# Kernel optimization log

Measured on AMD Instinct MI355X. Metric: run time of the kernel, lower is better.

Reference implementation:

```python
import jax, jax.numpy as jnp
from jax import lax
import numpy as np

B, L, D_MODEL = 4, 2048, 1024
D_STATE, D_CONV, EXPAND = 16, 4, 2
D_INNER = EXPAND * D_MODEL          # 2048
DT_RANK = D_MODEL // 16             # 64
LN_EPS = 1e-5


def setup_inputs() -> dict:
    key = jax.random.key(0)
    ks = jax.random.split(key, 8)
    s = 0.02
    # S4D-real init for A_log, as in Mamba
    A_init = jnp.tile(jnp.arange(1, D_STATE + 1, dtype=jnp.float32), (D_INNER, 1))
    return {
        "x": jax.random.normal(ks[0], (B, L, D_MODEL), jnp.float32),
        "ln_g": jnp.ones((D_MODEL,), jnp.float32),
        "ln_b": jnp.zeros((D_MODEL,), jnp.float32),
        "W_in": jax.random.normal(ks[1], (D_MODEL, 2 * D_INNER), jnp.float32) * s,
        "conv_w": jax.random.normal(ks[2], (D_INNER, D_CONV), jnp.float32) * s,
        "conv_b": jnp.zeros((D_INNER,), jnp.float32),
        "W_x": jax.random.normal(ks[3], (D_INNER, DT_RANK + 2 * D_STATE), jnp.float32) * s,
        "W_dt": jax.random.normal(ks[4], (DT_RANK, D_INNER), jnp.float32) * s,
        "b_dt": jnp.full((D_INNER,), -4.6, jnp.float32),  # softplus(b_dt) ~ 0.01
        "A_log": jnp.log(A_init),
        "Dskip": jnp.ones((D_INNER,), jnp.float32),
        "W_out": jax.random.normal(ks[5], (D_INNER, D_MODEL), jnp.float32) * s,
    }


def _layer_norm(x, g, b):
    mu = jnp.mean(x, -1, keepdims=True)
    var = jnp.mean((x - mu) ** 2, -1, keepdims=True)
    return (x - mu) * lax.rsqrt(var + LN_EPS) * g + b


def _mamba_block(x, ln_g, ln_b, W_in, conv_w, conv_b, W_x, W_dt, b_dt, A_log, Dskip, W_out):
    b, l, _ = x.shape
    xn = _layer_norm(x, ln_g, ln_b)

    # in_proj -> (u, z), each (B, L, d_inner)
    xz = xn @ W_in
    u, z = jnp.split(xz, 2, axis=-1)

    # causal depthwise conv over L + SiLU
    u_t = u.transpose(0, 2, 1)                      # (B, d_inner, L)
    k = conv_w[:, None, :]                          # (d_inner, 1, d_conv)
    uc = lax.conv_general_dilated(
        u_t, k, (1,), [(D_CONV - 1, 0)],
        dimension_numbers=("NCH", "OIH", "NCH"),
        feature_group_count=D_INNER,
    ) + conv_b[None, :, None]
    uc = jax.nn.silu(uc).transpose(0, 2, 1)         # (B, L, d_inner)

    # input-dependent dt, B, C
    dbc = uc @ W_x                                  # (B, L, dt_rank + 2*d_state)
    dt_r = dbc[..., :DT_RANK]
    Bs = dbc[..., DT_RANK:DT_RANK + D_STATE]        # (B, L, d_state)
    Cs = dbc[..., DT_RANK + D_STATE:]               # (B, L, d_state)
    dt = jax.nn.softplus(dt_r @ W_dt + b_dt)        # (B, L, d_inner)

    A = -jnp.exp(A_log)                             # (d_inner, d_state)

    def step(h, ins):
        dt_t, B_t, C_t, u_t = ins                   # (b,di),(b,ds),(b,ds),(b,di)
        dA = jnp.exp(dt_t[..., None] * A)           # (b, di, ds)
        h = h * dA + (dt_t * u_t)[..., None] * B_t[:, None, :]
        y = jnp.einsum("bds,bs->bd", h, C_t)
        return h, y

    h0 = jnp.zeros((b, D_INNER, D_STATE), x.dtype)
    xs = (dt.transpose(1, 0, 2), Bs.transpose(1, 0, 2),
          Cs.transpose(1, 0, 2), uc.transpose(1, 0, 2))
    _, ys = lax.scan(step, h0, xs)                  # (L, B, d_inner)
    y = ys.transpose(1, 0, 2) + uc * Dskip          # D skip connection
    y = y * jax.nn.silu(z)                          # gate
    return x + y @ W_out                            # residual (dropout=0)


def reference(x, ln_g, ln_b, W_in, conv_w, conv_b, W_x, W_dt, b_dt, A_log, Dskip, W_out):
    return _mamba_block(x, ln_g, ln_b, W_in, conv_w, conv_b, W_x, W_dt, b_dt, A_log, Dskip, W_out)
```

## Files before the change

### kernel.cpp

```cpp
#include <hip/hip_runtime.h>
#include <hip/hip_bf16.h>

#define BB 4
#define LL 2048
#define DM 1024
#define DI 2048
#define DST 16
#define DTR 64
#define ROWS (BB*LL)
#define NC 32
#define CHUNK (LL/NC)

using bf16x8 = __attribute__((ext_vector_type(8))) __bf16;
using f32x4  = __attribute__((ext_vector_type(4))) float;

#define AS1 __attribute__((address_space(1)))
#define AS3 __attribute__((address_space(3)))

__global__ __launch_bounds__(256) void transpose_all_kernel(
        const float* __restrict__ Wi, const float* __restrict__ Wo,
        const float* __restrict__ Wx, const float* __restrict__ Wd,
        __hip_bfloat16* __restrict__ WiT, __hip_bfloat16* __restrict__ WoT,
        __hip_bfloat16* __restrict__ WxT, __hip_bfloat16* __restrict__ WdT) {
    const int t = blockIdx.x;
    const float* src; __hip_bfloat16* dst; int R, C, Cpad, nx, idx;
    if (t < 4096)      { src = Wi; dst = WiT; R = 1024; C = 4096; Cpad = 4096; nx = 128; idx = t; }
    else if (t < 6144) { src = Wo; dst = WoT; R = 2048; C = 1024; Cpad = 1024; nx = 32;  idx = t - 4096; }
    else if (t < 6400) { src = Wx; dst = WxT; R = 2048; C = 96;   Cpad = 128;  nx = 4;   idx = t - 6144; }
    else               { src = Wd; dst = WdT; R = 64;   C = 2048; Cpad = 2048; nx = 64;  idx = t - 6400; }
    __shared__ float tl[32][33];
    const int c0 = (idx % nx) * 32, r0 = (idx / nx) * 32;
    const int tx = threadIdx.x & 31, ty = threadIdx.x >> 5;
    #pragma unroll
    for (int k = 0; k < 4; k++) {
        const int r = r0 + ty + 8 * k, c = c0 + tx;
        tl[ty + 8 * k][tx] = (r < R && c < C) ? src[(size_t)r * C + c] : 0.f;
    }
    __syncthreads();
    #pragma unroll
    for (int k = 0; k < 4; k++) {
        const int c = c0 + ty + 8 * k, r = r0 + tx;
        if (c < Cpad && r < R) dst[(size_t)c * R + r] = __float2bfloat16(tl[tx][ty + 8 * k]);
    }
}

__global__ __launch_bounds__(256) void ln_bf16_kernel(const float* __restrict__ x,
                                                      const float* __restrict__ g,
                                                      const float* __restrict__ bta,
                                                      __hip_bfloat16* __restrict__ xn) {
    const int row = blockIdx.x;
    const int tid = threadIdx.x;
    const float4 v = ((const float4*)(x + (size_t)row * DM))[tid];
    float s  = v.x + v.y + v.z + v.w;
    float sq = v.x*v.x + v.y*v.y + v.z*v.z + v.w*v.w;
    #pragma unroll
    for (int m = 1; m < 64; m <<= 1) {
        s  += __shfl_xor(s, m);
        sq += __shfl_xor(sq, m);
    }
    __shared__ float ss[4], ssq[4];
    const int w = tid >> 6;
    if ((tid & 63) == 0) { ss[w] = s; ssq[w] = sq; }
    __syncthreads();
    s  = ss[0] + ss[1] + ss[2] + ss[3];
    sq = ssq[0] + ssq[1] + ssq[2] + ssq[3];
    const float mu  = s * (1.f / DM);
    const float var = sq * (1.f / DM) - mu * mu;
    const float rs  = rsqrtf(var + 1e-5f);
    const float4 gv = ((const float4*)g)[tid];
    const float4 bv = ((const float4*)bta)[tid];
    __hip_bfloat16* op = xn + (size_t)row * DM + tid * 4;
    op[0] = __float2bfloat16((v.x - mu) * rs * gv.x + bv.x);
    op[1] = __float2bfloat16((v.y - mu) * rs * gv.y + bv.y);
    op[2] = __float2bfloat16((v.z - mu) * rs * gv.z + bv.z);
    op[3] = __float2bfloat16((v.w - mu) * rs * gv.w + bv.w);
}

template<int MODE>
__global__ __launch_bounds__(256) void mfma_gemm(const __hip_bfloat16* __restrict__ A,
                                                 const __hip_bfloat16* __restrict__ Bt,
                                                 float* __restrict__ O,
                                                 __hip_bfloat16* __restrict__ Oz,
                                                 __hip_bfloat16* __restrict__ Ozb,
                                                 const float* __restrict__ Add,
                                                 int Kstride, int klen) {
    __shared__ __hip_bfloat16 As[2 * 128 * 32];
    __shared__ __hip_bfloat16 Bs[2 * 128 * 32];
    const int tid  = threadIdx.x;
    const int lane = tid & 63;
    const int w    = tid >> 6;

    const int nbx = gridDim.x, nby = gridDim.y;
    const int lid = blockIdx.y * nbx + blockIdx.x;
    const int rpx = nby >> 3;
    const int xcd = lid & 7, sl = lid >> 3;
    const int by  = xcd * rpx + (sl % rpx);
    const int bx  = sl / rpx;

    const int row0 = by * 128, col0 = bx * 128;
    const int wr0 = (w >> 1) * 64, wc0 = (w & 1) * 64;

    f32x4 acc[4][4];
    #pragma unroll
    for (int i = 0; i < 4; i++)
        #pragma unroll
        for (int j = 0; j < 4; j++) acc[i][j] = f32x4{0.f, 0.f, 0.f, 0.f};

    const int fm  = lane & 15;
    const int fqi = lane >> 4;
    const int fqX = ((fqi ^ (fm & 3)) << 3);

    const int kbeg = blockIdx.z * klen;
    for (int k0 = kbeg; k0 < kbeg + klen; k0 += 64) {
        #pragma unroll
        for (int j = 0; j < 4; j++) {
            const int c   = w * 256 + j * 64 + lane;
            const int p   = c >> 9;
            const int row = (c >> 2) & 127;
            const int q   = (c & 3) ^ (row & 3);
            const int gk  = k0 + p * 32 + q * 8;
            __builtin_amdgcn_global_load_lds(
                (const AS1 unsigned int*)(A + (size_t)(row0 + row) * Kstride + gk),
                (AS3 unsigned int*)(As + c * 8), 16, 0, 0);
            __builtin_amdgcn_global_load_lds(
                (const AS1 unsigned int*)(Bt + (size_t)(col0 + row) * Kstride + gk),
                (AS3 unsigned int*)(Bs + c * 8), 16, 0, 0);
        }
        __syncthreads();
        #pragma unroll
        for (int half = 0; half < 2; half++) {
            bf16x8 af[4], bfr[4];
            #pragma unroll
            for (int i = 0; i < 4; i++)
                af[i] = *(const bf16x8*)&As[half * 4096 + (wr0 + i * 16 + fm) * 32 + fqX];
            #pragma unroll
            for (int j = 0; j < 4; j++)
                bfr[j] = *(const bf16x8*)&Bs[half * 4096 + (wc0 + j * 16 + fm) * 32 + fqX];
            #pragma unroll
            for (int i = 0; i < 4; i++)
                #pragma unroll
                for (int j = 0; j < 4; j++)
                    acc[i][j] = __builtin_amdgcn_mfma_f32_16x16x32_bf16(af[i], bfr[j], acc[i][j], 0, 0, 0);
        }
        __syncthreads();
    }

    #pragma unroll
    for (int i = 0; i < 4; i++) {
        #pragma unroll
        for (int j = 0; j < 4; j++) {
            #pragma unroll
            for (int r = 0; r < 4; r++) {
                const int row = row0 + wr0 + i * 16 + (lane >> 4) * 4 + r;
                const int col = col0 + wc0 + j * 16 + fm;
                const float v = acc[i][j][r];
                if (MODE == 2) {
                    O[(size_t)row * DM + col] = v + Add[(size_t)row * DM + col];
                } else if (MODE == 3) {
                    const float t  = v + Add[col];
                    const float sp = (t > 20.f) ? t : __logf(1.f + __expf(t));
                    Oz[(size_t)row * DI + col] = __float2bfloat16(sp);
                } else if (MODE == 4) {
                    O[((size_t)blockIdx.z * ROWS + row) * 128 + col] = v;
                }
            }
        }
    }
}

#define STAGE_A(buf, half, kt) do {                                              \
    _Pragma("unroll")                                                            \
    for (int j_ = 0; j_ < 2; j_++) {                                             \
        const int strip_ = w * 2 + j_;                                           \
        __builtin_amdgcn_global_load_lds(                                        \
            (const AS1 unsigned int*)(A + (size_t)(row0 + (half)*128 + strip_*8 + srow) * Kstride + ((kt)*64 + schk*8)), \
            (AS3 unsigned int*)(&As[buf][half][strip_*8][0] + sldo), 16, 0, 0);  \
    } } while (0)

#define STAGE_B(buf, half, kt) do {                                              \
    _Pragma("unroll")                                                            \
    for (int j_ = 0; j_ < 2; j_++) {                                             \
        const int strip_ = w * 2 + j_;                                           \
        __builtin_amdgcn_global_load_lds(                                        \
            (const AS1 unsigned int*)(Bt + (size_t)(col0 + (half)*128 + strip_*8 + srow) * Kstride + ((kt)*64 + schk*8)), \
            (AS3 unsigned int*)(&Bs[buf][half][strip_*8][0] + sldo), 16, 0, 0);  \
    } } while (0)

#define LOAD_A(buf, MH) do {                                                     \
    _Pragma("unroll")                                                            \
    for (int i_ = 0; i_ < 4; i_++) {                                             \
        const int r_ = (MH)*64 + i_*16 + fm;                                     \
        a_[i_][0] = *(const bf16x8*)&As[buf][wm][r_][((fq    ) ^ (fm & 7)) << 3];\
        a_[i_][1] = *(const bf16x8*)&As[buf][wm][r_][((fq + 4) ^ (fm & 7)) << 3];\
    } } while (0)

#define LOAD_B(dst, buf, NP) do {                                                \
    _Pragma("unroll")                                                            \
    for (int j_ = 0; j_ < 2; j_++) {                                             \
        const int c_ = (wn & 1)*64 + (NP)*32 + j_*16 + fm;                       \
        dst[j_][0] = *(const bf16x8*)&Bs[buf][wn >> 1][c_][((fq    ) ^ (fm & 7)) << 3]; \
        dst[j_][1] = *(const bf16x8*)&Bs[buf][wn >> 1][c_][((fq + 4) ^ (fm & 7)) << 3]; \
    } } while (0)

#define MFMA_Q(MH, NP, bset) do {                                                \
    __builtin_amdgcn_s_setprio(1);                                               \
    _Pragma("unroll")                                                            \
    for (int i_ = 0; i_ < 4; i_++)                                               \
        _Pragma("unroll")                                                        \
        for (int j_ = 0; j_ < 2; j_++) {                                         \
            acc[(MH)*4+i_][(NP)*2+j_] = __builtin_amdgcn_mfma_f32_16x16x32_bf16( \
                a_[i_][0], bset[j_][0], acc[(MH)*4+i_][(NP)*2+j_], 0, 0, 0);     \
            acc[(MH)*4+i_][(NP)*2+j_] = __builtin_amdgcn_mfma_f32_16x16x32_bf16( \
                a_[i_][1], bset[j_][1], acc[(MH)*4+i_][(NP)*2+j_], 0, 0, 0);     \
        }                                                                        \
    __builtin_amdgcn_s_setprio(0);                                               \
} while (0)

#define PH_SYNC() do {                                                           \
    __builtin_amdgcn_s_barrier();                                                \
    asm volatile("s_waitcnt lgkmcnt(0)" ::: "memory");                           \
} while (0)

#define TILE_BODY(BUF, OB, T) do {                                               \
               \
    LOAD_A(BUF, 0);                                                              \
    LOAD_B(b0_, BUF, 0);                                                         \
    if ((T) + 1 < nt) STAGE_B(OB, 1, (T) + 1);                                   \
    PH_SYNC();                                                                   \
    MFMA_Q(0, 0, b0_);                                                           \
    __builtin_amdgcn_s_barrier();                                                \
                                                                        \
    LOAD_B(b1_, BUF, 1);                                                         \
    PH_SYNC();                                                                   \
    MFMA_Q(0, 1, b1_);                                                           \
    __builtin_amdgcn_s_barrier();                                                \
               \
    LOAD_A(BUF, 1);                                                              \
    if ((T) + 2 < nt) STAGE_B(BUF, 0, (T) + 2);                                  \
    PH_SYNC();                                                                   \
    MFMA_Q(1, 1, b1_);                                                           \
    __builtin_amdgcn_s_barrier();                                                \
        \
    if ((T) + 2 < nt) { STAGE_A(BUF, 0, (T) + 2); STAGE_A(BUF, 1, (T) + 2); }    \
    MFMA_Q(1, 0, b0_);                                                           \
    if ((T) + 2 < nt) { asm volatile("s_waitcnt vmcnt(6)" ::: "memory"); }       \
    else              { asm volatile("s_waitcnt vmcnt(0)" ::: "memory"); }       \
    __builtin_amdgcn_s_barrier();                                                \
} while (0)

template<int MODE>
__global__ __launch_bounds__(512, 2) void mfma_gemm256(
        const __hip_bfloat16* __restrict__ A,
        const __hip_bfloat16* __restrict__ Bt,
        float* __restrict__ O,
        __hip_bfloat16* __restrict__ Oz,
        __hip_bfloat16* __restrict__ Ozb,
        const float* __restrict__ Add,
        int Kstride, int K) {
    __shared__ __hip_bfloat16 As[2][2][128][64];
    __shared__ __hip_bfloat16 Bs[2][2][128][64];
    const int tid  = threadIdx.x;
    const int lane = tid & 63;
    const int w    = tid >> 6;
    const int wm   = w >> 2;
    const int wn   = w & 3;
    const int fm   = lane & 15;
    const int fq   = lane >> 4;

    const int nbx = gridDim.x, nby = gridDim.y;
    const int lid = blockIdx.y * nbx + blockIdx.x;
    const int rpx = nby >> 3;
    const int xcd = lid & 7, sl = lid >> 3;
    const int by  = xcd * rpx + (sl % rpx);
    const int bx  = sl / rpx;
    const int row0 = by * 256, col0 = bx * 256;

    const int srow = lane >> 3;
    const int schk = (lane & 7) ^ srow;
    const int sldo = lane * 8;

    f32x4 acc[8][4];
    #pragma unroll
    for (int i = 0; i < 8; i++)
        #pragma unroll
        for (int j = 0; j < 4; j++) acc[i][j] = f32x4{0.f, 0.f, 0.f, 0.f};

    bf16x8 a_[4][2], b0_[2][2], b1_[2][2];

    STAGE_A(0, 0, 0); STAGE_A(0, 1, 0); STAGE_B(0, 0, 0); STAGE_B(0, 1, 0);
    STAGE_A(1, 0, 1); STAGE_A(1, 1, 1); STAGE_B(1, 0, 1);
    asm volatile("s_waitcnt vmcnt(6)" ::: "memory");
    __builtin_amdgcn_s_barrier();

    const int nt = K >> 6;
    for (int t = 0; t < nt; t += 2) {
        TILE_BODY(0, 1, t);
        TILE_BODY(1, 0, t + 1);
    }

    #pragma unroll
    for (int i = 0; i < 8; i++) {
        #pragma unroll
        for (int j = 0; j < 4; j++) {
            #pragma unroll
            for (int r = 0; r < 4; r++) {
                const int row = row0 + wm * 128 + i * 16 + fq * 4 + r;
                const int col = col0 + wn * 64 + j * 16 + fm;
                const float v = acc[i][j][r];
                if (MODE == 0) {
                    if (col0 < DI) Oz[(size_t)row * DI + col] = __float2bfloat16(v);
                    else           Ozb[(size_t)row * DI + (col - DI)] = __float2bfloat16(v);
                } else if (MODE == 2) {
                    O[(size_t)row * DM + col] = v + Add[(size_t)row * DM + col];
                }
            }
        }
    }
}
#undef STAGE_A
#undef STAGE_B
#undef LOAD_A
#undef LOAD_B
#undef MFMA_Q
#undef PH_SYNC
#undef TILE_BODY

__global__ __launch_bounds__(256) void dbc_reduce_kernel(const float* __restrict__ pbuf,
                                                         float* __restrict__ dbc,
                                                         __hip_bfloat16* __restrict__ dbc64) {
    const size_t gid = (size_t)blockIdx.x * 256 + threadIdx.x;
    const int    col = gid & 127;
    const size_t row = gid >> 7;
    float sum = 0.f;
    #pragma unroll
    for (int sp = 0; sp < 4; sp++)
        sum += pbuf[((size_t)sp * ROWS + row) * 128 + col];
    if (col < DTR)                   dbc64[row * DTR + col] = __float2bfloat16(sum);
    else if (col < DTR + 2 * DST)    dbc[row * 128 + col] = sum;
}

__global__ __launch_bounds__(256) void conv_silu_kernel(const __hip_bfloat16* __restrict__ u,
                                                        const float* __restrict__ cw,
                                                        const float* __restrict__ cb,
                                                        __hip_bfloat16* __restrict__ uc) {
    const int d  = blockIdx.x * 256 + threadIdx.x;
    const int b  = blockIdx.z;
    const int l0 = blockIdx.y * 16;
    const float w0 = cw[d * 4 + 0], w1 = cw[d * 4 + 1];
    const float w2 = cw[d * 4 + 2], w3 = cw[d * 4 + 3];
    const float bias = cb[d];
    const __hip_bfloat16* up = u + (size_t)(b * LL) * DI + d;
    float x0 = (l0 - 3 >= 0) ? __bfloat162float(up[(size_t)(l0 - 3) * DI]) : 0.f;
    float x1 = (l0 - 2 >= 0) ? __bfloat162float(up[(size_t)(l0 - 2) * DI]) : 0.f;
    float x2 = (l0 - 1 >= 0) ? __bfloat162float(up[(size_t)(l0 - 1) * DI]) : 0.f;
    __hip_bfloat16* op = uc + (size_t)(b * LL + l0) * DI + d;
    #pragma unroll
    for (int i = 0; i < 16; i++) {
        const float x3 = __bfloat162float(up[(size_t)(l0 + i) * DI]);
        const float v  = bias + w0 * x0 + w1 * x1 + w2 * x2 + w3 * x3;
        const float sig = __builtin_amdgcn_rcpf(1.f + __expf(-v));
        op[(size_t)i * DI] = __float2bfloat16(v * sig);
        x0 = x1; x1 = x2; x2 = x3;
    }
}

__global__ __launch_bounds__(256) void scan_pass1_kernel(const __hip_bfloat16* __restrict__ dtb,
                                                         const __hip_bfloat16* __restrict__ uc,
                                                         const float* __restrict__ dbc,
                                                         const float* __restrict__ A_log,
                                                         float* __restrict__ hbuf,
                                                         float* __restrict__ Pbuf) {
    __shared__ float Bsh[CHUNK][16];
    const int tid = threadIdx.x;
    const int d   = blockIdx.x * 256 + tid;
    const int c   = blockIdx.y;
    const int b   = blockIdx.z;
    const size_t row0 = (size_t)b * LL + (size_t)c * CHUNK;

    {
        const int r = tid >> 2, j4 = (tid & 3) * 4;
        *(float4*)&Bsh[r][j4] = *(const float4*)(dbc + (row0 + r) * 128 + DTR + j4);
    }
    float a[DST];
    #pragma unroll
    for (int q = 0; q < 4; q++) {
        const float4 t = *(const float4*)(A_log + (size_t)d * DST + q * 4);
        a[q * 4 + 0] = -__expf(t.x); a[q * 4 + 1] = -__expf(t.y);
        a[q * 4 + 2] = -__expf(t.z); a[q * 4 + 3] = -__expf(t.w);
    }
    __syncthreads();

    const __hip_bfloat16* dtp = dtb + row0 * DI + d;
    const __hip_bfloat16* ucp = uc + row0 * DI + d;

    float h[DST];
    #pragma unroll
    for (int s = 0; s < DST; s++) h[s] = 0.f;
    float sdt = 0.f;
    float dtv = __bfloat162float(dtp[0]), ucv = __bfloat162float(ucp[0]);
    for (int l = 0; l < CHUNK; l++) {
        const int ln = (l + 1 < CHUNK) ? (l + 1) : l;
        const float dtn = __bfloat162float(dtp[(size_t)ln * DI]);
        const float ucn = __bfloat162float(ucp[(size_t)ln * DI]);
        const float dtu = dtv * ucv;
        sdt += dtv;
        #pragma unroll
        for (int s = 0; s < DST; s++) {
            const float dA = __expf(dtv * a[s]);
            h[s] = fmaf(h[s], dA, dtu * Bsh[l][s]);
        }
        dtv = dtn; ucv = ucn;
    }
    float* hp = hbuf + (((size_t)b * NC + c) * DI + d) * DST;
    float* pp = Pbuf + (((size_t)b * NC + c) * DI + d) * DST;
    #pragma unroll
    for (int q = 0; q < 4; q++) {
        *(float4*)&hp[q * 4] = float4{h[q*4+0], h[q*4+1], h[q*4+2], h[q*4+3]};
        *(float4*)&pp[q * 4] = float4{__expf(sdt * a[q*4+0]), __expf(sdt * a[q*4+1]),
                                      __expf(sdt * a[q*4+2]), __expf(sdt * a[q*4+3])};
    }
}

__global__ __launch_bounds__(256) void scan_combine_kernel(float* __restrict__ hbuf,
                                                           const float* __restrict__ Pbuf) {
    const size_t gid  = (size_t)blockIdx.x * 256 + threadIdx.x;
    const size_t b    = gid >> 15;
    const size_t d16s = gid & 32767;
    float H = 0.f;
    #pragma unroll
    for (int c = 0; c < NC; c++) {
        const size_t idx = (b * NC + c) * (DI * DST) + d16s;
        const float hc = hbuf[idx];
        const float Pc = Pbuf[idx];
        hbuf[idx] = H;
        H = hc + Pc * H;
    }
}

__global__ __launch_bounds__(256) void scan_pass3_kernel(const __hip_bfloat16* __restrict__ dtb,
                                                         __hip_bfloat16* uc,
                                                         const __hip_bfloat16* __restrict__ z,
                                                         const float* __restrict__ dbc,
                                                         const float* __restrict__ A_log,
                                                         const float* __restrict__ Dskip,
                                                         const float* __restrict__ hbuf) {
    __shared__ float BC[CHUNK][32];
    const int tid = threadIdx.x;
    const int d   = blockIdx.x * 256 + tid;
    const int c   = blockIdx.y;
    const int b   = blockIdx.z;
    const size_t row0 = (size_t)b * LL + (size_t)c * CHUNK;

    #pragma unroll
    for (int i = 0; i < 2; i++) {
        const int idx = i * 256 + tid;
        const int r = idx >> 3, j4 = (idx & 7) * 4;
        *(float4*)&BC[r][j4] = *(const float4*)(dbc + (row0 + r) * 128 + DTR + j4);
    }
    float a[DST];
    #pragma unroll
    for (int q = 0; q < 4; q++) {
        const float4 t = *(const float4*)(A_log + (size_t)d * DST + q * 4);
        a[q * 4 + 0] = -__expf(t.x); a[q * 4 + 1] = -__expf(t.y);
        a[q * 4 + 2] = -__expf(t.z); a[q * 4 + 3] = -__expf(t.w);
    }
    const float dsk = Dskip[d];
    __syncthreads();

    const __hip_bfloat16* dtp = dtb + row0 * DI + d;
    __hip_bfloat16* ucp = uc + row0 * DI + d;
    const __hip_bfloat16* zp = z + row0 * DI + d;

    float h[DST];
    {
        const float* hp = hbuf + (((size_t)b * NC + c) * DI + d) * DST;
        #pragma unroll
        for (int q = 0; q < 4; q++) {
            const float4 t = *(const float4*)&hp[q * 4];
            h[q*4+0] = t.x; h[q*4+1] = t.y; h[q*4+2] = t.z; h[q*4+3] = t.w;
        }
    }
    float dtv = __bfloat162float(dtp[0]);
    float ucv = __bfloat162float(ucp[0]);
    float zv  = __bfloat162float(zp[0]);
    for (int l = 0; l < CHUNK; l++) {
        const int ln = (l + 1 < CHUNK) ? (l + 1) : l;
        const float dtn = __bfloat162float(dtp[(size_t)ln * DI]);
        const float ucn = __bfloat162float(ucp[(size_t)ln * DI]);
        const float zn  = __bfloat162float(zp[(size_t)ln * DI]);
        const float dtu = dtv * ucv;
        float y = 0.f;
        #pragma unroll
        for (int s = 0; s < DST; s++) {
            const float dA = __expf(dtv * a[s]);
            h[s] = fmaf(h[s], dA, dtu * BC[l][s]);
            y = fmaf(h[s], BC[l][16 + s], y);
        }
        const float yt  = fmaf(ucv, dsk, y);
        const float sig = __builtin_amdgcn_rcpf(1.f + __expf(-zv));
        ucp[(size_t)l * DI] = __float2bfloat16(yt * (zv * sig));
        dtv = dtn; ucv = ucn; zv = zn;
    }
}

extern "C" void kernel_launch(void* const* d_in, const int* in_sizes, int n_in,
                              void* d_out, int out_size, void* d_ws, size_t ws_size,
                              hipStream_t stream) {
    const float* x      = (const float*)d_in[0];
    const float* ln_g   = (const float*)d_in[1];
    const float* ln_b   = (const float*)d_in[2];
    const float* W_in   = (const float*)d_in[3];
    const float* conv_w = (const float*)d_in[4];
    const float* conv_b = (const float*)d_in[5];
    const float* W_x    = (const float*)d_in[6];
    const float* W_dt   = (const float*)d_in[7];
    const float* b_dt   = (const float*)d_in[8];
    const float* A_log  = (const float*)d_in[9];
    const float* Dskip  = (const float*)d_in[10];
    const float* W_out  = (const float*)d_in[11];
    float* out = (float*)d_out;

    const size_t MB = 1024ull * 1024ull;
    char* wsb = (char*)d_ws;
    __hip_bfloat16* ub    = (__hip_bfloat16*)(wsb);
    __hip_bfloat16* z     = (__hip_bfloat16*)(wsb + 32 * MB);
    __hip_bfloat16* uc    = (__hip_bfloat16*)(wsb + 64 * MB);
    __hip_bfloat16* xn    = (__hip_bfloat16*)(wsb + 96 * MB);
    __hip_bfloat16* WinT  = (__hip_bfloat16*)(wsb + 112 * MB);
    __hip_bfloat16* WoutT = (__hip_bfloat16*)(wsb + 120 * MB);
    __hip_bfloat16* WxT   = (__hip_bfloat16*)(wsb + 124 * MB);
    float*          dbc   = (float*)(wsb + 125 * MB);
    float*          hbuf  = (float*)(wsb + 129 * MB);
    float*          Pbuf  = (float*)(wsb + 145 * MB);
    __hip_bfloat16* dbc64 = (__hip_bfloat16*)(wsb + 161 * MB);
    __hip_bfloat16* WdtT  = (__hip_bfloat16*)(wsb + 162 * MB);
    float*          pbuf  = (float*)(wsb + 163 * MB);
    __hip_bfloat16* dtb   = ub;

    transpose_all_kernel<<<6528, 256, 0, stream>>>(W_in, W_out, W_x, W_dt,
                                                   WinT, WoutT, WxT, WdtT);
    ln_bf16_kernel<<<ROWS, 256, 0, stream>>>(x, ln_g, ln_b, xn);
    mfma_gemm256<0><<<dim3(16, 32), 512, 0, stream>>>(
        xn, WinT, nullptr, ub, z, nullptr, DM, DM);
    conv_silu_kernel<<<dim3(DI / 256, LL / 16, BB), 256, 0, stream>>>(ub, conv_w, conv_b, uc);
    mfma_gemm<4><<<dim3(1, 64, 4), 256, 0, stream>>>(
        uc, WxT, pbuf, nullptr, nullptr, nullptr, DI, DI / 4);
    dbc_reduce_kernel<<<(ROWS * 128) / 256, 256, 0, stream>>>(pbuf, dbc, dbc64);
    mfma_gemm<3><<<dim3(DI / 128, ROWS / 128), 256, 0, stream>>>(
        dbc64, WdtT, nullptr, dtb, nullptr, b_dt, DTR, DTR);
    scan_pass1_kernel<<<dim3(DI / 256, NC, BB), 256, 0, stream>>>(dtb, uc, dbc, A_log, hbuf, Pbuf);
    scan_combine_kernel<<<(BB * DI * DST) / 256, 256, 0, stream>>>(hbuf, Pbuf);
    scan_pass3_kernel<<<dim3(DI / 256, NC, BB), 256, 0, stream>>>(dtb, uc, z, dbc, A_log, Dskip, hbuf);
    mfma_gemm<2><<<dim3(DM / 128, ROWS / 128), 256, 0, stream>>>(
        uc, WoutT, out, nullptr, nullptr, x, DI, DI);
}
```

Measured before the change: 422.2 us.

## Fuse causal conv+SiLU into dbc GEMM and scan passes; merge LayerNorm into prep

```diff
diff --git a/kernel.cpp b/kernel.cpp
--- a/kernel.cpp
+++ b/kernel.cpp
@@ -17,12 +17,49 @@
 #define AS1 __attribute__((address_space(1)))
 #define AS3 __attribute__((address_space(3)))
 
-__global__ __launch_bounds__(256) void transpose_all_kernel(
+static __device__ __forceinline__ float bf2f(__bf16 v) {
+    unsigned short s = __builtin_bit_cast(unsigned short, v);
+    unsigned int   u = (unsigned int)s << 16;
+    return __builtin_bit_cast(float, u);
+}
+
+__global__ __launch_bounds__(256) void prep_kernel(
+        const float* __restrict__ x, const float* __restrict__ g,
+        const float* __restrict__ bta, __hip_bfloat16* __restrict__ xn,
         const float* __restrict__ Wi, const float* __restrict__ Wo,
         const float* __restrict__ Wx, const float* __restrict__ Wd,
         __hip_bfloat16* __restrict__ WiT, __hip_bfloat16* __restrict__ WoT,
         __hip_bfloat16* __restrict__ WxT, __hip_bfloat16* __restrict__ WdT) {
-    const int t = blockIdx.x;
+    if (blockIdx.x < ROWS) {
+        const int row = blockIdx.x;
+        const int tid = threadIdx.x;
+        const float4 v = ((const float4*)(x + (size_t)row * DM))[tid];
+        float s  = v.x + v.y + v.z + v.w;
+        float sq = v.x*v.x + v.y*v.y + v.z*v.z + v.w*v.w;
+        #pragma unroll
+        for (int m = 1; m < 64; m <<= 1) {
+            s  += __shfl_xor(s, m);
+            sq += __shfl_xor(sq, m);
+        }
+        __shared__ float ss[4], ssq[4];
+        const int w = tid >> 6;
+        if ((tid & 63) == 0) { ss[w] = s; ssq[w] = sq; }
+        __syncthreads();
+        s  = ss[0] + ss[1] + ss[2] + ss[3];
+        sq = ssq[0] + ssq[1] + ssq[2] + ssq[3];
+        const float mu  = s * (1.f / DM);
+        const float var = sq * (1.f / DM) - mu * mu;
+        const float rs  = rsqrtf(var + 1e-5f);
+        const float4 gv = ((const float4*)g)[tid];
+        const float4 bv = ((const float4*)bta)[tid];
+        __hip_bfloat16* op = xn + (size_t)row * DM + tid * 4;
+        op[0] = __float2bfloat16((v.x - mu) * rs * gv.x + bv.x);
+        op[1] = __float2bfloat16((v.y - mu) * rs * gv.y + bv.y);
+        op[2] = __float2bfloat16((v.z - mu) * rs * gv.z + bv.z);
+        op[3] = __float2bfloat16((v.w - mu) * rs * gv.w + bv.w);
+        return;
+    }
+    const int t = blockIdx.x - ROWS;
     const float* src; __hip_bfloat16* dst; int R, C, Cpad, nx, idx;
     if (t < 4096)      { src = Wi; dst = WiT; R = 1024; C = 4096; Cpad = 4096; nx = 128; idx = t; }
     else if (t < 6144) { src = Wo; dst = WoT; R = 2048; C = 1024; Cpad = 1024; nx = 32;  idx = t - 4096; }
@@ -42,38 +79,6 @@
         const int c = c0 + ty + 8 * k, r = r0 + tx;
         if (c < Cpad && r < R) dst[(size_t)c * R + r] = __float2bfloat16(tl[tx][ty + 8 * k]);
     }
-}
-
-__global__ __launch_bounds__(256) void ln_bf16_kernel(const float* __restrict__ x,
-                                                      const float* __restrict__ g,
-                                                      const float* __restrict__ bta,
-                                                      __hip_bfloat16* __restrict__ xn) {
-    const int row = blockIdx.x;
-    const int tid = threadIdx.x;
-    const float4 v = ((const float4*)(x + (size_t)row * DM))[tid];
-    float s  = v.x + v.y + v.z + v.w;
-    float sq = v.x*v.x + v.y*v.y + v.z*v.z + v.w*v.w;
-    #pragma unroll
-    for (int m = 1; m < 64; m <<= 1) {
-        s  += __shfl_xor(s, m);
-        sq += __shfl_xor(sq, m);
-    }
-    __shared__ float ss[4], ssq[4];
-    const int w = tid >> 6;
-    if ((tid & 63) == 0) { ss[w] = s; ssq[w] = sq; }
-    __syncthreads();
-    s  = ss[0] + ss[1] + ss[2] + ss[3];
-    sq = ssq[0] + ssq[1] + ssq[2] + ssq[3];
-    const float mu  = s * (1.f / DM);
-    const float var = sq * (1.f / DM) - mu * mu;
-    const float rs  = rsqrtf(var + 1e-5f);
-    const float4 gv = ((const float4*)g)[tid];
-    const float4 bv = ((const float4*)bta)[tid];
-    __hip_bfloat16* op = xn + (size_t)row * DM + tid * 4;
-    op[0] = __float2bfloat16((v.x - mu) * rs * gv.x + bv.x);
-    op[1] = __float2bfloat16((v.y - mu) * rs * gv.y + bv.y);
-    op[2] = __float2bfloat16((v.z - mu) * rs * gv.z + bv.z);
-    op[3] = __float2bfloat16((v.w - mu) * rs * gv.w + bv.w);
 }
 
 template<int MODE>
@@ -160,9 +165,102 @@
                     const float t  = v + Add[col];
                     const float sp = (t > 20.f) ? t : __logf(1.f + __expf(t));
                     Oz[(size_t)row * DI + col] = __float2bfloat16(sp);
-                } else if (MODE == 4) {
-                    O[((size_t)blockIdx.z * ROWS + row) * 128 + col] = v;
                 }
+            }
+        }
+    }
+}
+
+__global__ __launch_bounds__(256) void gemm_dbc_kernel(const __hip_bfloat16* __restrict__ ub,
+                                                       const __hip_bfloat16* __restrict__ Bt,
+                                                       const float* __restrict__ cw,
+                                                       const float* __restrict__ cb,
+                                                       float* __restrict__ O) {
+    __shared__ __hip_bfloat16 As[2 * 128 * 32];
+    __shared__ __hip_bfloat16 Bs[2 * 128 * 32];
+    const int tid  = threadIdx.x;
+    const int lane = tid & 63;
+    const int w    = tid >> 6;
+
+    const int nby = gridDim.y;
+    const int lid = blockIdx.y;
+    const int rpx = nby >> 3;
+    const int xcd = lid & 7, sl = lid >> 3;
+    const int by  = xcd * rpx + (sl % rpx);
+    const int row0 = by * 128;
+    const int wr0 = (w >> 1) * 64, wc0 = (w & 1) * 64;
+
+    f32x4 acc[4][4];
+    #pragma unroll
+    for (int i = 0; i < 4; i++)
+        #pragma unroll
+        for (int j = 0; j < 4; j++) acc[i][j] = f32x4{0.f, 0.f, 0.f, 0.f};
+
+    const int fm  = lane & 15;
+    const int fqi = lane >> 4;
+    const int fqX = ((fqi ^ (fm & 3)) << 3);
+
+    const int klen = DI / 4;
+    const int kbeg = blockIdx.z * klen;
+    for (int k0 = kbeg; k0 < kbeg + klen; k0 += 64) {
+        #pragma unroll
+        for (int j = 0; j < 4; j++) {
+            const int c   = w * 256 + j * 64 + lane;
+            const int p   = c >> 9;
+            const int row = (c >> 2) & 127;
+            const int q   = (c & 3) ^ (row & 3);
+            const int gk  = k0 + p * 32 + q * 8;
+            __builtin_amdgcn_global_load_lds(
+                (const AS1 unsigned int*)(Bt + (size_t)row * DI + gk),
+                (AS3 unsigned int*)(Bs + c * 8), 16, 0, 0);
+            const int grow = row0 + row;
+            const int l    = grow & (LL - 1);
+            const size_t base = (size_t)grow * DI + gk;
+            bf16x8 x3v = *(const bf16x8*)(ub + base);
+            bf16x8 x0v{}, x1v{}, x2v{};
+            if (l >= 3) x0v = *(const bf16x8*)(ub + base - (size_t)3 * DI);
+            if (l >= 2) x1v = *(const bf16x8*)(ub + base - (size_t)2 * DI);
+            if (l >= 1) x2v = *(const bf16x8*)(ub + base - (size_t)1 * DI);
+            alignas(16) __hip_bfloat16 o8[8];
+            #pragma unroll
+            for (int e = 0; e < 8; e++) {
+                const int d = gk + e;
+                const float4 wv = *(const float4*)(cw + d * 4);
+                const float v = cb[d] + wv.x * bf2f(x0v[e]) + wv.y * bf2f(x1v[e])
+                                      + wv.z * bf2f(x2v[e]) + wv.w * bf2f(x3v[e]);
+                const float sig = __builtin_amdgcn_rcpf(1.f + __expf(-v));
+                o8[e] = __float2bfloat16(v * sig);
+            }
+            *(bf16x8*)&As[c * 8] = *(const bf16x8*)o8;
+        }
+        __syncthreads();
+        #pragma unroll
+        for (int half = 0; half < 2; half++) {
+            bf16x8 af[4], bfr[4];
+            #pragma unroll
+            for (int i = 0; i < 4; i++)
+                af[i] = *(const bf16x8*)&As[half * 4096 + (wr0 + i * 16 + fm) * 32 + fqX];
+            #pragma unroll
+            for (int j = 0; j < 4; j++)
+                bfr[j] = *(const bf16x8*)&Bs[half * 4096 + (wc0 + j * 16 + fm) * 32 + fqX];
+            #pragma unroll
+            for (int i = 0; i < 4; i++)
+                #pragma unroll
+                for (int j = 0; j < 4; j++)
+                    acc[i][j] = __builtin_amdgcn_mfma_f32_16x16x32_bf16(af[i], bfr[j], acc[i][j], 0, 0, 0);
+        }
+        __syncthreads();
+    }
+
+    #pragma unroll
+    for (int i = 0; i < 4; i++) {
+        #pragma unroll
+        for (int j = 0; j < 4; j++) {
+            #pragma unroll
+            for (int r = 0; r < 4; r++) {
+                const int row = row0 + wr0 + i * 16 + (lane >> 4) * 4 + r;
+                const int col = wc0 + j * 16 + fm;
+                O[((size_t)blockIdx.z * ROWS + row) * 128 + col] = acc[i][j][r];
             }
         }
     }
@@ -222,25 +320,21 @@
 } while (0)
 
 #define TILE_BODY(BUF, OB, T) do {                                               \
-               \
     LOAD_A(BUF, 0);                                                              \
     LOAD_B(b0_, BUF, 0);                                                         \
     if ((T) + 1 < nt) STAGE_B(OB, 1, (T) + 1);                                   \
     PH_SYNC();                                                                   \
     MFMA_Q(0, 0, b0_);                                                           \
     __builtin_amdgcn_s_barrier();                                                \
-                                                                        \
     LOAD_B(b1_, BUF, 1);                                                         \
     PH_SYNC();                                                                   \
     MFMA_Q(0, 1, b1_);                                                           \
     __builtin_amdgcn_s_barrier();                                                \
-               \
     LOAD_A(BUF, 1);                                                              \
     if ((T) + 2 < nt) STAGE_B(BUF, 0, (T) + 2);                                  \
     PH_SYNC();                                                                   \
     MFMA_Q(1, 1, b1_);                                                           \
     __builtin_amdgcn_s_barrier();                                                \
-        \
     if ((T) + 2 < nt) { STAGE_A(BUF, 0, (T) + 2); STAGE_A(BUF, 1, (T) + 2); }    \
     MFMA_Q(1, 0, b0_);                                                           \
     if ((T) + 2 < nt) { asm volatile("s_waitcnt vmcnt(6)" ::: "memory"); }       \
@@ -339,33 +433,10 @@
     else if (col < DTR + 2 * DST)    dbc[row * 128 + col] = sum;
 }
 
-__global__ __launch_bounds__(256) void conv_silu_kernel(const __hip_bfloat16* __restrict__ u,
-                                                        const float* __restrict__ cw,
-                                                        const float* __restrict__ cb,
-                                                        __hip_bfloat16* __restrict__ uc) {
-    const int d  = blockIdx.x * 256 + threadIdx.x;
-    const int b  = blockIdx.z;
-    const int l0 = blockIdx.y * 16;
-    const float w0 = cw[d * 4 + 0], w1 = cw[d * 4 + 1];
-    const float w2 = cw[d * 4 + 2], w3 = cw[d * 4 + 3];
-    const float bias = cb[d];
-    const __hip_bfloat16* up = u + (size_t)(b * LL) * DI + d;
-    float x0 = (l0 - 3 >= 0) ? __bfloat162float(up[(size_t)(l0 - 3) * DI]) : 0.f;
-    float x1 = (l0 - 2 >= 0) ? __bfloat162float(up[(size_t)(l0 - 2) * DI]) : 0.f;
-    float x2 = (l0 - 1 >= 0) ? __bfloat162float(up[(size_t)(l0 - 1) * DI]) : 0.f;
-    __hip_bfloat16* op = uc + (size_t)(b * LL + l0) * DI + d;
-    #pragma unroll
-    for (int i = 0; i < 16; i++) {
-        const float x3 = __bfloat162float(up[(size_t)(l0 + i) * DI]);
-        const float v  = bias + w0 * x0 + w1 * x1 + w2 * x2 + w3 * x3;
-        const float sig = __builtin_amdgcn_rcpf(1.f + __expf(-v));
-        op[(size_t)i * DI] = __float2bfloat16(v * sig);
-        x0 = x1; x1 = x2; x2 = x3;
-    }
-}
-
 __global__ __launch_bounds__(256) void scan_pass1_kernel(const __hip_bfloat16* __restrict__ dtb,
-                                                         const __hip_bfloat16* __restrict__ uc,
+                                                         const __hip_bfloat16* __restrict__ ub,
+                                                         const float* __restrict__ cw,
+                                                         const float* __restrict__ cb,
                                                          const float* __restrict__ dbc,
                                                          const float* __restrict__ A_log,
                                                          float* __restrict__ hbuf,
@@ -381,43 +452,55 @@
         const int r = tid >> 2, j4 = (tid & 3) * 4;
         *(float4*)&Bsh[r][j4] = *(const float4*)(dbc + (row0 + r) * 128 + DTR + j4);
     }
-    float a[DST];
+    float a2[DST];
     #pragma unroll
     for (int q = 0; q < 4; q++) {
         const float4 t = *(const float4*)(A_log + (size_t)d * DST + q * 4);
-        a[q * 4 + 0] = -__expf(t.x); a[q * 4 + 1] = -__expf(t.y);
-        a[q * 4 + 2] = -__expf(t.z); a[q * 4 + 3] = -__expf(t.w);
-    }
+        a2[q * 4 + 0] = -__expf(t.x) * 1.44269504f;
+        a2[q * 4 + 1] = -__expf(t.y) * 1.44269504f;
+        a2[q * 4 + 2] = -__expf(t.z) * 1.44269504f;
+        a2[q * 4 + 3] = -__expf(t.w) * 1.44269504f;
+    }
+    const float4 wv  = *(const float4*)(cw + d * 4);
+    const float bias = cb[d];
     __syncthreads();
 
     const __hip_bfloat16* dtp = dtb + row0 * DI + d;
-    const __hip_bfloat16* ucp = uc + row0 * DI + d;
+    const __hip_bfloat16* up  = ub + ((size_t)b * LL) * DI + d;
+    const int l0 = c * CHUNK;
+
+    float xw0 = (l0 >= 3) ? __bfloat162float(up[(size_t)(l0 - 3) * DI]) : 0.f;
+    float xw1 = (l0 >= 2) ? __bfloat162float(up[(size_t)(l0 - 2) * DI]) : 0.f;
+    float xw2 = (l0 >= 1) ? __bfloat162float(up[(size_t)(l0 - 1) * DI]) : 0.f;
+    float x3  = __bfloat162float(up[(size_t)l0 * DI]);
 
     float h[DST];
     #pragma unroll
     for (int s = 0; s < DST; s++) h[s] = 0.f;
     float sdt = 0.f;
-    float dtv = __bfloat162float(dtp[0]), ucv = __bfloat162float(ucp[0]);
+    float dtv = __bfloat162float(dtp[0]);
     for (int l = 0; l < CHUNK; l++) {
         const int ln = (l + 1 < CHUNK) ? (l + 1) : l;
         const float dtn = __bfloat162float(dtp[(size_t)ln * DI]);
-        const float ucn = __bfloat162float(ucp[(size_t)ln * DI]);
+        const float x3n = __bfloat162float(up[(size_t)(l0 + ln) * DI]);
+        const float v   = bias + wv.x * xw0 + wv.y * xw1 + wv.z * xw2 + wv.w * x3;
+        const float ucv = v * __builtin_amdgcn_rcpf(1.f + __expf(-v));
         const float dtu = dtv * ucv;
         sdt += dtv;
         #pragma unroll
         for (int s = 0; s < DST; s++) {
-            const float dA = __expf(dtv * a[s]);
+            const float dA = exp2f(dtv * a2[s]);
             h[s] = fmaf(h[s], dA, dtu * Bsh[l][s]);
         }
-        dtv = dtn; ucv = ucn;
+        xw0 = xw1; xw1 = xw2; xw2 = x3; x3 = x3n; dtv = dtn;
     }
     float* hp = hbuf + (((size_t)b * NC + c) * DI + d) * DST;
     float* pp = Pbuf + (((size_t)b * NC + c) * DI + d) * DST;
     #pragma unroll
     for (int q = 0; q < 4; q++) {
         *(float4*)&hp[q * 4] = float4{h[q*4+0], h[q*4+1], h[q*4+2], h[q*4+3]};
-        *(float4*)&pp[q * 4] = float4{__expf(sdt * a[q*4+0]), __expf(sdt * a[q*4+1]),
-                                      __expf(sdt * a[q*4+2]), __expf(sdt * a[q*4+3])};
+        *(float4*)&pp[q * 4] = float4{exp2f(sdt * a2[q*4+0]), exp2f(sdt * a2[q*4+1]),
+                                      exp2f(sdt * a2[q*4+2]), exp2f(sdt * a2[q*4+3])};
     }
 }
 
@@ -438,12 +521,15 @@
 }
 
 __global__ __launch_bounds__(256) void scan_pass3_kernel(const __hip_bfloat16* __restrict__ dtb,
-                                                         __hip_bfloat16* uc,
+                                                         const __hip_bfloat16* __restrict__ ub,
                                                          const __hip_bfloat16* __restrict__ z,
+                                                         const float* __restrict__ cw,
+                                                         const float* __restrict__ cb,
                                                          const float* __restrict__ dbc,
                                                          const float* __restrict__ A_log,
                                                          const float* __restrict__ Dskip,
-                                                         const float* __restrict__ hbuf) {
+                                                         const float* __restrict__ hbuf,
+                                                         __hip_bfloat16* __restrict__ yg) {
     __shared__ float BC[CHUNK][32];
     const int tid = threadIdx.x;
     const int d   = blockIdx.x * 256 + tid;
@@ -457,19 +543,25 @@
         const int r = idx >> 3, j4 = (idx & 7) * 4;
         *(float4*)&BC[r][j4] = *(const float4*)(dbc + (row0 + r) * 128 + DTR + j4);
     }
-    float a[DST];
+    float a2[DST];
     #pragma unroll
     for (int q = 0; q < 4; q++) {
         const float4 t = *(const float4*)(A_log + (size_t)d * DST + q * 4);
-        a[q * 4 + 0] = -__expf(t.x); a[q * 4 + 1] = -__expf(t.y);
-        a[q * 4 + 2] = -__expf(t.z); a[q * 4 + 3] = -__expf(t.w);
-    }
-    const float dsk = Dskip[d];
+        a2[q * 4 + 0] = -__expf(t.x) * 1.44269504f;
+        a2[q * 4 + 1] = -__expf(t.y) * 1.44269504f;
+        a2[q * 4 + 2] = -__expf(t.z) * 1.44269504f;
+        a2[q * 4 + 3] = -__expf(t.w) * 1.44269504f;
+    }
+    const float4 wv  = *(const float4*)(cw + d * 4);
+    const float bias = cb[d];
+    const float dsk  = Dskip[d];
     __syncthreads();
 
     const __hip_bfloat16* dtp = dtb + row0 * DI + d;
-    __hip_bfloat16* ucp = uc + row0 * DI + d;
-    const __hip_bfloat16* zp = z + row0 * DI + d;
+    const __hip_bfloat16* up  = ub + ((size_t)b * LL) * DI + d;
+    const __hip_bfloat16* zp  = z + row0 * DI + d;
+    __hip_bfloat16* ygp = yg + row0 * DI + d;
+    const int l0 = c * CHUNK;
 
     float h[DST];
     {
@@ -480,26 +572,31 @@
             h[q*4+0] = t.x; h[q*4+1] = t.y; h[q*4+2] = t.z; h[q*4+3] = t.w;
         }
     }
+    float xw0 = (l0 >= 3) ? __bfloat162float(up[(size_t)(l0 - 3) * DI]) : 0.f;
+    float xw1 = (l0 >= 2) ? __bfloat162float(up[(size_t)(l0 - 2) * DI]) : 0.f;
+    float xw2 = (l0 >= 1) ? __bfloat162float(up[(size_t)(l0 - 1) * DI]) : 0.f;
+    float x3  = __bfloat162float(up[(size_t)l0 * DI]);
     float dtv = __bfloat162float(dtp[0]);
-    float ucv = __bfloat162float(ucp[0]);
     float zv  = __bfloat162float(zp[0]);
     for (int l = 0; l < CHUNK; l++) {
         const int ln = (l + 1 < CHUNK) ? (l + 1) : l;
         const float dtn = __bfloat162float(dtp[(size_t)ln * DI]);
-        const float ucn = __bfloat162float(ucp[(size_t)ln * DI]);
+        const float x3n = __bfloat162float(up[(size_t)(l0 + ln) * DI]);
         const float zn  = __bfloat162float(zp[(size_t)ln * DI]);
+        const float v   = bias + wv.x * xw0 + wv.y * xw1 + wv.z * xw2 + wv.w * x3;
+        const float ucv = v * __builtin_amdgcn_rcpf(1.f + __expf(-v));
         const float dtu = dtv * ucv;
         float y = 0.f;
         #pragma unroll
         for (int s = 0; s < DST; s++) {
-            const float dA = __expf(dtv * a[s]);
+            const float dA = exp2f(dtv * a2[s]);
             h[s] = fmaf(h[s], dA, dtu * BC[l][s]);
             y = fmaf(h[s], BC[l][16 + s], y);
         }
         const float yt  = fmaf(ucv, dsk, y);
         const float sig = __builtin_amdgcn_rcpf(1.f + __expf(-zv));
-        ucp[(size_t)l * DI] = __float2bfloat16(yt * (zv * sig));
-        dtv = dtn; ucv = ucn; zv = zn;
+        ygp[(size_t)l * DI] = __float2bfloat16(yt * (zv * sig));
+        xw0 = xw1; xw1 = xw2; xw2 = x3; x3 = x3n; dtv = dtn; zv = zn;
     }
 }
 
@@ -524,7 +621,7 @@
     char* wsb = (char*)d_ws;
     __hip_bfloat16* ub    = (__hip_bfloat16*)(wsb);
     __hip_bfloat16* z     = (__hip_bfloat16*)(wsb + 32 * MB);
-    __hip_bfloat16* uc    = (__hip_bfloat16*)(wsb + 64 * MB);
+    __hip_bfloat16* yg    = (__hip_bfloat16*)(wsb + 64 * MB);
     __hip_bfloat16* xn    = (__hip_bfloat16*)(wsb + 96 * MB);
     __hip_bfloat16* WinT  = (__hip_bfloat16*)(wsb + 112 * MB);
     __hip_bfloat16* WoutT = (__hip_bfloat16*)(wsb + 120 * MB);
@@ -535,22 +632,22 @@
     __hip_bfloat16* dbc64 = (__hip_bfloat16*)(wsb + 161 * MB);
     __hip_bfloat16* WdtT  = (__hip_bfloat16*)(wsb + 162 * MB);
     float*          pbuf  = (float*)(wsb + 163 * MB);
-    __hip_bfloat16* dtb   = ub;
-
-    transpose_all_kernel<<<6528, 256, 0, stream>>>(W_in, W_out, W_x, W_dt,
-                                                   WinT, WoutT, WxT, WdtT);
-    ln_bf16_kernel<<<ROWS, 256, 0, stream>>>(x, ln_g, ln_b, xn);
+    __hip_bfloat16* dtb   = (__hip_bfloat16*)(wsb + 163 * MB);
+
+    prep_kernel<<<ROWS + 6528, 256, 0, stream>>>(x, ln_g, ln_b, xn,
+                                                 W_in, W_out, W_x, W_dt,
+                                                 WinT, WoutT, WxT, WdtT);
     mfma_gemm256<0><<<dim3(16, 32), 512, 0, stream>>>(
         xn, WinT, nullptr, ub, z, nullptr, DM, DM);
-    conv_silu_kernel<<<dim3(DI / 256, LL / 16, BB), 256, 0, stream>>>(ub, conv_w, conv_b, uc);
-    mfma_gemm<4><<<dim3(1, 64, 4), 256, 0, stream>>>(
-        uc, WxT, pbuf, nullptr, nullptr, nullptr, DI, DI / 4);
+    gemm_dbc_kernel<<<dim3(1, 64, 4), 256, 0, stream>>>(ub, WxT, conv_w, conv_b, pbuf);
     dbc_reduce_kernel<<<(ROWS * 128) / 256, 256, 0, stream>>>(pbuf, dbc, dbc64);
     mfma_gemm<3><<<dim3(DI / 128, ROWS / 128), 256, 0, stream>>>(
         dbc64, WdtT, nullptr, dtb, nullptr, b_dt, DTR, DTR);
-    scan_pass1_kernel<<<dim3(DI / 256, NC, BB), 256, 0, stream>>>(dtb, uc, dbc, A_log, hbuf, Pbuf);
+    scan_pass1_kernel<<<dim3(DI / 256, NC, BB), 256, 0, stream>>>(
+        dtb, ub, conv_w, conv_b, dbc, A_log, hbuf, Pbuf);
     scan_combine_kernel<<<(BB * DI * DST) / 256, 256, 0, stream>>>(hbuf, Pbuf);
-    scan_pass3_kernel<<<dim3(DI / 256, NC, BB), 256, 0, stream>>>(dtb, uc, z, dbc, A_log, Dskip, hbuf);
+    scan_pass3_kernel<<<dim3(DI / 256, NC, BB), 256, 0, stream>>>(
+        dtb, ub, z, conv_w, conv_b, dbc, A_log, Dskip, hbuf, yg);
     mfma_gemm<2><<<dim3(DM / 128, ROWS / 128), 256, 0, stream>>>(
-        uc, WoutT, out, nullptr, nullptr, x, DI, DI);
-}
+        yg, WoutT, out, nullptr, nullptr, x, DI, DI);
+}
```

Measured after the change: 526.0 us. 24.6% more time.
